# Kernel tuning notes

Measured on AMD Instinct MI355X. Metric: run time of the kernel, lower is better.

## Reference

```python
import jax, jax.numpy as jnp
import numpy as np

IN_FEATURES = 8192
OUT_FEATURES = 8192
CODESZ = 8            # E8 lattice dimension per code index
CODEBOOK_SIZE = 65536 # 2^16-entry codebook (16-bit indices)
TOKENS = 32           # decode-style batch


def fwht(x):
    """Fast Walsh-Hadamard transform (Sylvester order) along the last axis.
    n must be a power of 2. Unnormalized (multiply by H_n)."""
    n = x.shape[-1]
    steps = int(np.log2(n))
    h = 1
    for _ in range(steps):
        y = x.reshape(*x.shape[:-1], n // (2 * h), 2, h)
        a = y[..., 0, :]
        b = y[..., 1, :]
        x = jnp.stack([a + b, a - b], axis=-2).reshape(*y.shape[:-3], n)
        h *= 2
    return x


def setup_inputs() -> dict:
    key = jax.random.key(0)
    k0, k1, k2, k3, k4 = jax.random.split(key, 5)
    x = jax.random.normal(k0, (TOKENS, IN_FEATURES), dtype=jnp.float32)
    # learned codebook: CODEBOOK_SIZE vectors of CODESZ entries (E8P-like lattice points)
    codebook_table = jax.random.normal(k1, (CODEBOOK_SIZE, CODESZ), dtype=jnp.float32) * 0.1
    # quantized weight indices: [out_features, in_features // codesz]
    Qidxs = jax.random.randint(k2, (OUT_FEATURES, IN_FEATURES // CODESZ), 0, CODEBOOK_SIZE, dtype=jnp.int32)
    # random sign vectors (incoherence processing)
    SU = (2.0 * jax.random.randint(k3, (IN_FEATURES,), 0, 2) - 1.0).astype(jnp.float32)
    SV = (2.0 * jax.random.randint(k4, (OUT_FEATURES,), 0, 2) - 1.0).astype(jnp.float32)
    Wscale = jnp.array(0.02, dtype=jnp.float32)
    return {"x": x, "codebook_table": codebook_table, "Qidxs": Qidxs,
            "SU": SU, "SV": SV, "Wscale": Wscale}


def reference(x, codebook_table, Qidxs, SU, SV, Wscale):
    n_in = x.shape[-1]
    n_out = SV.shape[0]
    # input incoherence: sign flip then orthonormal Hadamard rotation (matmul_hadUt)
    xh = fwht(x * SU) * (1.0 / jnp.sqrt(jnp.float32(n_in)))  # [T, n_in]
    # codebook dequantization: gather lattice vectors and lay out as [n_out, n_in]
    W = codebook_table[Qidxs].reshape(n_out, n_in)
    # quantized matmul in the rotated basis
    z = xh @ W.T  # [T, n_out]
    # output rotation (matmul_hadU) + sign/scale (SV absorbs Wscale in the torch code)
    out = fwht(z) * (1.0 / jnp.sqrt(jnp.float32(n_out))) * (SV * Wscale)
    return out
```

## Files before the change

kernel.cpp:

```cpp
#include <hip/hip_runtime.h>
#include <hip/hip_bf16.h>


typedef __attribute__((ext_vector_type(16))) float f32x16;
typedef __attribute__((ext_vector_type(8))) __bf16 bf16x8;
typedef __attribute__((ext_vector_type(4))) __bf16 bf16x4;
typedef __attribute__((ext_vector_type(4))) int i32x4;

#define IN_F 8192
#define OUT_F 8192
#define TOKENS 32
#define KSPLIT 8
#define KCHUNK 1024
#define CH (KCHUNK / 8)
#define GROUPS (KCHUNK / 32)
#define DG 5
#define DI 7
#define INV_SQRT_8192 0.011048543456039806f
#define PAD(i) ((i) + ((i) >> 5))

#if __has_builtin(__builtin_amdgcn_raw_buffer_load_b128) && \
    __has_builtin(__builtin_amdgcn_make_buffer_rsrc)
#define HAVE_BUF 1
#else
#define HAVE_BUF 0
#endif

__device__ inline void h4_reg(float v[4]) {
    float t0 = v[0] + v[1], t1 = v[0] - v[1];
    float t2 = v[2] + v[3], t3 = v[2] - v[3];
    v[0] = t0 + t2; v[1] = t1 + t3; v[2] = t0 - t2; v[3] = t1 - t3;
}

__device__ inline void fwht1024(float v[4], float* st, int tid) {
    h4_reg(v);
    const int lane = tid & 63;
    #pragma unroll
    for (int m = 1; m < 64; m <<= 1) {
        #pragma unroll
        for (int j = 0; j < 4; ++j) {
            float p = __shfl_xor(v[j], m, 64);
            v[j] = (lane & m) ? (p - v[j]) : (v[j] + p);
        }
    }
    #pragma unroll
    for (int j = 0; j < 4; ++j) st[PAD(4 * tid + j)] = v[j];
    __syncthreads();
    #pragma unroll
    for (int j = 0; j < 4; ++j) v[j] = st[PAD(tid + j * 256)];
    h4_reg(v);
}

__global__ __launch_bounds__(256)
void prep_kernel(const float* __restrict__ cb, __bf16* __restrict__ cbb,
                 const float* __restrict__ x, const float* __restrict__ su,
                 __bf16* __restrict__ xh) {
    __shared__ float st[1056];
    const int tid = threadIdx.x;
    if (blockIdx.x < 512) {
        int i = blockIdx.x * 256 + tid;
        float4 vv = ((const float4*)cb)[i];
        bf16x4 o;
        o[0] = (__bf16)vv.x; o[1] = (__bf16)vv.y;
        o[2] = (__bf16)vv.z; o[3] = (__bf16)vv.w;
        ((bf16x4*)cbb)[i] = o;
        return;
    }
    const int id = blockIdx.x - 512;
    const int t = id >> 3, ch = id & 7;
    float sgn[8];
    #pragma unroll
    for (int k = 0; k < 8; ++k)
        sgn[k] = (__builtin_popcount(ch & k) & 1) ? -1.f : 1.f;
    float v[4] = {0.f, 0.f, 0.f, 0.f};
    #pragma unroll
    for (int k = 0; k < 8; ++k) {
        float4 xv = *(const float4*)(x + (size_t)t * IN_F + k * 1024 + tid * 4);
        float4 s4 = *(const float4*)(su + k * 1024 + tid * 4);
        v[0] += sgn[k] * xv.x * s4.x;
        v[1] += sgn[k] * xv.y * s4.y;
        v[2] += sgn[k] * xv.z * s4.z;
        v[3] += sgn[k] * xv.w * s4.w;
    }
    fwht1024(v, st, tid);
    __bf16* dst = xh + (size_t)t * IN_F + ch * 1024;
    #pragma unroll
    for (int j = 0; j < 4; ++j)
        dst[tid + j * 256] = (__bf16)(v[j] * INV_SQRT_8192);
}

__global__ __launch_bounds__(512, 4)
void qgemm_kernel(const int* __restrict__ qidxs,
                  const __bf16* __restrict__ cb,
                  const __bf16* __restrict__ xh,
                  __bf16* __restrict__ zpart) {
    __shared__ __align__(16) __bf16 xt[TOKENS * KCHUNK];
    const int ks = blockIdx.x & (KSPLIT - 1);
    const int nb = blockIdx.x >> 3;
    const int tid = threadIdx.x;
    const int wave = tid >> 6, lane = tid & 63;
    const int h = lane >> 5, lc = lane & 31;
    const int n = nb * 256 + wave * 32 + lc;

    #pragma unroll
    for (int i = 0; i < 8; ++i) {
        int f = i * 512 + tid, r = f >> 7, c = f & 127;
        i32x4 v = *(const i32x4*)(xh + (size_t)r * IN_F + ks * KCHUNK + c * 8);
        *(i32x4*)(xt + ((r * CH + (c ^ (r & 7))) << 3)) = v;
    }
    __syncthreads();

    const int* qrow = qidxs + (size_t)n * (IN_F / 8) + ks * (KCHUNK / 8);

#if HAVE_BUF
    __amdgpu_buffer_rsrc_t rsrc = __builtin_amdgcn_make_buffer_rsrc(
        (void*)cb, (short)0, 65536 * 16, 0x00020000);
    #define GA(ix, au) __builtin_bit_cast(bf16x8, \
        __builtin_amdgcn_raw_buffer_load_b128(rsrc, (ix) << 4, 0, au))
#else
    const bf16x8* cbv = (const bf16x8*)cb;
    #define GA(ix, au) (cbv[ix])
#endif

    f32x16 acc;
    #pragma unroll
    for (int i = 0; i < 16; ++i) acc[i] = 0.f;

    i32x4 iv[GROUPS];
    bf16x8 bfr[GROUPS][2];

    #pragma unroll
    for (int g = 0; g < DI; ++g)
        iv[g] = *(const i32x4*)(qrow + g * 4);
    #pragma unroll
    for (int g = 0; g < DG; ++g) {
        if (g & 1) {
            bfr[g][0] = GA(h ? iv[g][1] : iv[g][0], 1);
            bfr[g][1] = GA(h ? iv[g][3] : iv[g][2], 1);
        } else {
            bfr[g][0] = GA(h ? iv[g][1] : iv[g][0], 0);
            bfr[g][1] = GA(h ? iv[g][3] : iv[g][2], 0);
        }
    }

    #pragma unroll
    for (int g = 0; g < GROUPS; ++g) {
        if (g + DI < GROUPS)
            iv[g + DI] = *(const i32x4*)(qrow + (g + DI) * 4);
        if (g + DG < GROUPS) {
            if ((g + DG) & 1) {
                bfr[g + DG][0] = GA(h ? iv[g + DG][1] : iv[g + DG][0], 1);
                bfr[g + DG][1] = GA(h ? iv[g + DG][3] : iv[g + DG][2], 1);
            } else {
                bfr[g + DG][0] = GA(h ? iv[g + DG][1] : iv[g + DG][0], 0);
                bfr[g + DG][1] = GA(h ? iv[g + DG][3] : iv[g + DG][2], 0);
            }
        }
        #pragma unroll
        for (int sgi = 0; sgi < 2; ++sgi) {
            const int T = 2 * g + sgi;
            bf16x8 a = *(const bf16x8*)(xt +
                          ((lc * CH + ((2 * T + h) ^ (lc & 7))) << 3));
            acc = __builtin_amdgcn_mfma_f32_32x32x16_bf16(a, bfr[g][sgi],
                                                          acc, 0, 0, 0);
        }
    }

    __bf16* zp = zpart + ((size_t)ks * TOKENS) * OUT_F + n;
    #pragma unroll
    for (int r = 0; r < 16; ++r) {
        int m = (r & 3) + 4 * h + 8 * (r >> 2);
        zp[(size_t)m * OUT_F] = (__bf16)acc[r];
    }
}

__global__ __launch_bounds__(256)
void zsumA_kernel(const __bf16* __restrict__ zpart, float* __restrict__ z1) {
    __shared__ float st[1056];
    const int tid = threadIdx.x;
    const int t = blockIdx.x >> 3, ch = blockIdx.x & 7;
    float v[4] = {0.f, 0.f, 0.f, 0.f};
    #pragma unroll
    for (int ks = 0; ks < KSPLIT; ++ks) {
        bf16x4 b = *(const bf16x4*)(zpart +
                     ((size_t)(ks * TOKENS + t)) * OUT_F + ch * 1024 + tid * 4);
        v[0] += (float)b[0]; v[1] += (float)b[1];
        v[2] += (float)b[2]; v[3] += (float)b[3];
    }
    fwht1024(v, st, tid);
    float* dst = z1 + (size_t)t * OUT_F + ch * 1024;
    #pragma unroll
    for (int j = 0; j < 4; ++j)
        dst[tid + j * 256] = v[j];
}

__global__ __launch_bounds__(256)
void zsumB_kernel(const float* __restrict__ z1, const float* __restrict__ sv,
                  const float* __restrict__ wscale, float* __restrict__ out) {
    const int id = blockIdx.x * 256 + threadIdx.x;
    const int t = id >> 10, c = id & 1023;
    float v[8];
    #pragma unroll
    for (int k = 0; k < 8; ++k)
        v[k] = z1[t * OUT_F + k * 1024 + c];
    #pragma unroll
    for (int h = 1; h < 8; h <<= 1)
        #pragma unroll
        for (int i = 0; i < 8; i += 2 * h)
            #pragma unroll
            for (int j = 0; j < h; ++j) {
                float a = v[i + j], b = v[i + j + h];
                v[i + j] = a + b;
                v[i + j + h] = a - b;
            }
    const float sc = INV_SQRT_8192 * wscale[0];
    #pragma unroll
    for (int k = 0; k < 8; ++k)
        out[t * OUT_F + k * 1024 + c] = v[k] * sc * sv[k * 1024 + c];
}

extern "C" void kernel_launch(void* const* d_in, const int* in_sizes, int n_in,
                              void* d_out, int out_size, void* d_ws, size_t ws_size,
                              hipStream_t stream) {
    const float* x      = (const float*)d_in[0];
    const float* cb     = (const float*)d_in[1];
    const int*   qidxs  = (const int*)d_in[2];
    const float* su     = (const float*)d_in[3];
    const float* sv     = (const float*)d_in[4];
    const float* wscale = (const float*)d_in[5];
    float* out = (float*)d_out;

    char* ws = (char*)d_ws;
    __bf16* cbb   = (__bf16*)ws;
    __bf16* xh    = (__bf16*)(ws + (1u << 20));
    __bf16* zpart = (__bf16*)(ws + (1u << 20) + (512u << 10));
    float*  z1    = (float*)(ws + (5u << 20) + (512u << 10));

    hipLaunchKernelGGL(prep_kernel, dim3(768), dim3(256), 0, stream,
                       cb, cbb, x, su, xh);
    hipLaunchKernelGGL(qgemm_kernel, dim3(32 * KSPLIT), dim3(512), 0, stream,
                       qidxs, cbb, xh, zpart);
    hipLaunchKernelGGL(zsumA_kernel, dim3(256), dim3(256), 0, stream,
                       zpart, z1);
    hipLaunchKernelGGL(zsumB_kernel, dim3(128), dim3(256), 0, stream,
                       z1, sv, wscale, out);
}
```

Measured before the change: 127.8 us.

## Reduce split-K partials with float atomics and fuse output Hadamard into one kernel

The qgemm kernel now accumulates split-K partials straight into a zeroed fp32 buffer with atomicAdd, replacing the bf16 partial store. The prep kernel zeroes that buffer. The two post-GEMM kernels are merged into one that folds the 8-way outer Hadamard stage into the load via sign patterns, then runs the 1024-point FWHT and applies scale and SV. This removes one kernel launch, the partial-sum traffic and an intermediate buffer. In exchange it adds atomic contention (8 adds per output) and a nondeterministic summation order.

Result: no change. 127.7 us (-0.0%).

```diff
diff --git a/kernel.cpp b/kernel.cpp
--- a/kernel.cpp
+++ b/kernel.cpp
@@ -54,7 +54,7 @@
 __global__ __launch_bounds__(256)
 void prep_kernel(const float* __restrict__ cb, __bf16* __restrict__ cbb,
                  const float* __restrict__ x, const float* __restrict__ su,
-                 __bf16* __restrict__ xh) {
+                 __bf16* __restrict__ xh, float* __restrict__ z) {
     __shared__ float st[1056];
     const int tid = threadIdx.x;
     if (blockIdx.x < 512) {
@@ -64,6 +64,7 @@
         o[0] = (__bf16)vv.x; o[1] = (__bf16)vv.y;
         o[2] = (__bf16)vv.z; o[3] = (__bf16)vv.w;
         ((bf16x4*)cbb)[i] = o;
+        ((float2*)z)[i] = make_float2(0.f, 0.f);
         return;
     }
     const int id = blockIdx.x - 512;
@@ -93,7 +94,7 @@
 void qgemm_kernel(const int* __restrict__ qidxs,
                   const __bf16* __restrict__ cb,
                   const __bf16* __restrict__ xh,
-                  __bf16* __restrict__ zpart) {
+                  float* __restrict__ z) {
     __shared__ __align__(16) __bf16 xt[TOKENS * KCHUNK];
     const int ks = blockIdx.x & (KSPLIT - 1);
     const int nb = blockIdx.x >> 3;
@@ -166,57 +167,39 @@
         }
     }
 
-    __bf16* zp = zpart + ((size_t)ks * TOKENS) * OUT_F + n;
     #pragma unroll
     for (int r = 0; r < 16; ++r) {
         int m = (r & 3) + 4 * h + 8 * (r >> 2);
-        zp[(size_t)m * OUT_F] = (__bf16)acc[r];
+        atomicAdd(z + (size_t)m * OUT_F + n, acc[r]);
     }
 }
 
 __global__ __launch_bounds__(256)
-void zsumA_kernel(const __bf16* __restrict__ zpart, float* __restrict__ z1) {
+void zsum_kernel(const float* __restrict__ z, const float* __restrict__ sv,
+                 const float* __restrict__ wscale, float* __restrict__ out) {
     __shared__ float st[1056];
     const int tid = threadIdx.x;
     const int t = blockIdx.x >> 3, ch = blockIdx.x & 7;
+    float sgn[8];
+    #pragma unroll
+    for (int k = 0; k < 8; ++k)
+        sgn[k] = (__builtin_popcount(ch & k) & 1) ? -1.f : 1.f;
     float v[4] = {0.f, 0.f, 0.f, 0.f};
     #pragma unroll
-    for (int ks = 0; ks < KSPLIT; ++ks) {
-        bf16x4 b = *(const bf16x4*)(zpart +
-                     ((size_t)(ks * TOKENS + t)) * OUT_F + ch * 1024 + tid * 4);
-        v[0] += (float)b[0]; v[1] += (float)b[1];
-        v[2] += (float)b[2]; v[3] += (float)b[3];
+    for (int kk = 0; kk < 8; ++kk) {
+        float4 zv = *(const float4*)(z + (size_t)t * OUT_F + kk * 1024 + tid * 4);
+        v[0] += sgn[kk] * zv.x;
+        v[1] += sgn[kk] * zv.y;
+        v[2] += sgn[kk] * zv.z;
+        v[3] += sgn[kk] * zv.w;
     }
     fwht1024(v, st, tid);
-    float* dst = z1 + (size_t)t * OUT_F + ch * 1024;
+    const float sc = INV_SQRT_8192 * wscale[0];
+    float* dst = out + (size_t)t * OUT_F + ch * 1024;
+    const float* svp = sv + ch * 1024;
     #pragma unroll
     for (int j = 0; j < 4; ++j)
-        dst[tid + j * 256] = v[j];
-}
-
-__global__ __launch_bounds__(256)
-void zsumB_kernel(const float* __restrict__ z1, const float* __restrict__ sv,
-                  const float* __restrict__ wscale, float* __restrict__ out) {
-    const int id = blockIdx.x * 256 + threadIdx.x;
-    const int t = id >> 10, c = id & 1023;
-    float v[8];
-    #pragma unroll
-    for (int k = 0; k < 8; ++k)
-        v[k] = z1[t * OUT_F + k * 1024 + c];
-    #pragma unroll
-    for (int h = 1; h < 8; h <<= 1)
-        #pragma unroll
-        for (int i = 0; i < 8; i += 2 * h)
-            #pragma unroll
-            for (int j = 0; j < h; ++j) {
-                float a = v[i + j], b = v[i + j + h];
-                v[i + j] = a + b;
-                v[i + j + h] = a - b;
-            }
-    const float sc = INV_SQRT_8192 * wscale[0];
-    #pragma unroll
-    for (int k = 0; k < 8; ++k)
-        out[t * OUT_F + k * 1024 + c] = v[k] * sc * sv[k * 1024 + c];
+        dst[tid + j * 256] = v[j] * sc * svp[tid + j * 256];
 }
 
 extern "C" void kernel_launch(void* const* d_in, const int* in_sizes, int n_in,
@@ -231,17 +214,14 @@
     float* out = (float*)d_out;
 
     char* ws = (char*)d_ws;
-    __bf16* cbb   = (__bf16*)ws;
-    __bf16* xh    = (__bf16*)(ws + (1u << 20));
-    __bf16* zpart = (__bf16*)(ws + (1u << 20) + (512u << 10));
-    float*  z1    = (float*)(ws + (5u << 20) + (512u << 10));
+    __bf16* cbb = (__bf16*)ws;
+    __bf16* xh  = (__bf16*)(ws + (1u << 20));
+    float*  z   = (float*)(ws + (1u << 20) + (512u << 10));
 
     hipLaunchKernelGGL(prep_kernel, dim3(768), dim3(256), 0, stream,
-                       cb, cbb, x, su, xh);
+                       cb, cbb, x, su, xh, z);
     hipLaunchKernelGGL(qgemm_kernel, dim3(32 * KSPLIT), dim3(512), 0, stream,
-                       qidxs, cbb, xh, zpart);
-    hipLaunchKernelGGL(zsumA_kernel, dim3(256), dim3(256), 0, stream,
-                       zpart, z1);
-    hipLaunchKernelGGL(zsumB_kernel, dim3(128), dim3(256), 0, stream,
-                       z1, sv, wscale, out);
-}
+                       qidxs, cbb, xh, z);
+    hipLaunchKernelGGL(zsum_kernel, dim3(256), dim3(256), 0, stream,
+                       z, sv, wscale, out);
+}
```
